# Optimization experiments

Measured on AMD Instinct MI355X. Metric: run time of the kernel, lower is better.

Reference implementation:

```python
import jax, jax.numpy as jnp
import numpy as np

N, E, F, H = 50000, 500000, 128, 128   # nodes, edges, in-features, hidden
L, R, B = 3, 8, 30                     # layers, relations, bases
G, C = 16, 8                           # graphs in batch, classes
EPS = 1e-5


def setup_inputs() -> dict:
    key = jax.random.key(0)
    ks = jax.random.split(key, 16)
    x = jax.random.normal(ks[0], (N, F), jnp.float32)
    edge_index = jax.random.randint(ks[1], (2, E), 0, N)
    edge_attr = jax.random.randint(ks[2], (E,), 0, R)
    batch = jnp.sort(jax.random.randint(ks[3], (N,), 0, G))
    # RGCN params (all layers share shapes since F == H)
    basis = jax.random.normal(ks[4], (L, B, H, H), jnp.float32) * 0.05
    comp = jax.random.normal(ks[5], (L, R, B), jnp.float32) * 0.2
    root = jax.random.normal(ks[6], (L, H, H), jnp.float32) * 0.05
    bias = jnp.zeros((L, H), jnp.float32)
    # BatchNorm (eval mode: running stats)
    bn1_gamma = jnp.ones((F,), jnp.float32)
    bn1_beta = jnp.zeros((F,), jnp.float32)
    bn1_mean = jax.random.normal(ks[7], (F,), jnp.float32) * 0.1
    bn1_var = jax.random.uniform(ks[8], (F,), jnp.float32, 0.5, 1.5)
    bn2_gamma = jnp.ones((H,), jnp.float32)
    bn2_beta = jnp.zeros((H,), jnp.float32)
    bn2_mean = jax.random.normal(ks[9], (H,), jnp.float32) * 0.1
    bn2_var = jax.random.uniform(ks[10], (H,), jnp.float32, 0.5, 1.5)
    fc1_w = jax.random.normal(ks[11], (H, H), jnp.float32) * 0.05
    fc1_b = jnp.zeros((H,), jnp.float32)
    fc2_w = jax.random.normal(ks[12], (H, C), jnp.float32) * 0.05
    fc2_b = jnp.zeros((C,), jnp.float32)
    return dict(x=x, edge_index=edge_index, edge_attr=edge_attr, batch=batch,
                bn1_gamma=bn1_gamma, bn1_beta=bn1_beta, bn1_mean=bn1_mean, bn1_var=bn1_var,
                basis=basis, comp=comp, root=root, bias=bias,
                bn2_gamma=bn2_gamma, bn2_beta=bn2_beta, bn2_mean=bn2_mean, bn2_var=bn2_var,
                fc1_w=fc1_w, fc1_b=fc1_b, fc2_w=fc2_w, fc2_b=fc2_b)


def _bn(x, gamma, beta, mean, var):
    return (x - mean) * jax.lax.rsqrt(var + EPS) * gamma + beta


def _rgcn_layer(x, basis_l, comp_l, root_l, bias_l, src, dst, edge_attr):
    # root transform + bias
    out = x @ root_l + bias_l
    # relation-wise basis-decomposed message passing, mean-aggregated per relation
    for r in range(R):
        W_r = jnp.einsum('b,bio->io', comp_l[r], basis_l)  # [H, H]
        xw = x @ W_r                                       # [N, H]
        mask = (edge_attr == r).astype(x.dtype)            # [E]
        msg = xw[src] * mask[:, None]                      # gather + mask
        agg = jax.ops.segment_sum(msg, dst, num_segments=N)
        deg = jax.ops.segment_sum(mask, dst, num_segments=N)
        out = out + agg / jnp.maximum(deg, 1.0)[:, None]
    return out


def reference(x, edge_index, edge_attr, batch,
              bn1_gamma, bn1_beta, bn1_mean, bn1_var,
              basis, comp, root, bias,
              bn2_gamma, bn2_beta, bn2_mean, bn2_var,
              fc1_w, fc1_b, fc2_w, fc2_b):
    src, dst = edge_index[0], edge_index[1]
    h = _bn(x, bn1_gamma, bn1_beta, bn1_mean, bn1_var)
    for l in range(L):
        h = jax.nn.relu(_rgcn_layer(h, basis[l], comp[l], root[l], bias[l], src, dst, edge_attr))
        # dropout is identity in eval mode
    # global mean pool per graph
    sums = jax.ops.segment_sum(h, batch, num_segments=G)            # [G, H]
    counts = jax.ops.segment_sum(jnp.ones((N,), h.dtype), batch, num_segments=G)
    g = sums / jnp.maximum(counts, 1.0)[:, None]
    g = _bn(g, bn2_gamma, bn2_beta, bn2_mean, bn2_var)
    # temporal_type == 'mean'
    v = jax.nn.relu(g.mean(axis=0))                                 # [H]
    v = jax.nn.relu(v @ fc1_w + fc1_b)
    logits = v @ fc2_w + fc2_b                                      # [C]
    return jax.nn.log_softmax(logits, axis=-1)
```

## Files before the change

### kernel.cpp

```cpp
#include <hip/hip_runtime.h>
#include <hip/hip_bf16.h>

#define NN 50000
#define NE 500000
#define HID 128
#define LAYERS 3
#define RELS 8
#define BASES 30
#define GRAPHS 16
#define CLASSES 8
#define EPSV 1e-5f
#define NOUT (HID * (RELS + 1))
#define SCAN_CHUNK 1024
#define SCAN_NBLK ((NN + SCAN_CHUNK - 1) / SCAN_CHUNK)
#define PCHUNK 128
#define NSTRIPE ((NN + 127) / 128)
#define NSG ((NSTRIPE + 7) / 8)

typedef __attribute__((ext_vector_type(8))) short short8;
typedef __attribute__((ext_vector_type(4))) float f32x4;
typedef __attribute__((ext_vector_type(2))) float f32x2;

__device__ __forceinline__ float bf2f(unsigned short u) {
    union { unsigned int i; float f; } x; x.i = ((unsigned int)u) << 16; return x.f;
}
__device__ __forceinline__ unsigned short f2bf(float f) {
    __hip_bfloat16 b = __float2bfloat16(f);
    return *(unsigned short*)&b;
}
template <bool HI>
__device__ __forceinline__ f32x2 fp8x2_2f(int u) {
    return __builtin_amdgcn_cvt_pk_f32_fp8(u, HI);
}
__device__ __forceinline__ int permf(int f) {
    return (f & 64) | ((f & 15) << 2) | ((f >> 4) & 3);
}
__device__ __forceinline__ int ipermf(int q) {
    return (q & 64) | ((q & 3) << 4) | ((q >> 2) & 15);
}
__device__ __forceinline__ void gload16(const void* g, void* l) {
    __builtin_amdgcn_global_load_lds(
        (const __attribute__((address_space(1))) unsigned int*)g,
        (__attribute__((address_space(3))) unsigned int*)l, 16, 0, 0);
}

__global__ __launch_bounds__(256) void build_wcat(const float* __restrict__ basis,
                                                  const float* __restrict__ comp,
                                                  const float* __restrict__ root,
                                                  unsigned short* __restrict__ wT) {
    int bid = blockIdx.x;
    int l = bid >> 6;
    int k0 = (bid & 63) << 1;
    __shared__ float cl[RELS * BASES];
    int tid = threadIdx.x;
    if (tid < RELS * BASES) cl[tid] = comp[l * RELS * BASES + tid];
    __syncthreads();
    int j = tid & 127;
    int k = k0 + (tid >> 7);
    int pk = permf(k);
    const float* bp = basis + ((size_t)l * BASES * HID + k) * HID + j;
    float acc[RELS];
#pragma unroll
    for (int r = 0; r < RELS; ++r) acc[r] = 0.f;
    for (int b = 0; b < BASES; ++b) {
        float v = bp[(size_t)b * HID * HID];
#pragma unroll
        for (int r = 0; r < RELS; ++r) acc[r] += cl[r * BASES + b] * v;
    }
    unsigned short* wl = wT + (size_t)l * NOUT * HID;
#pragma unroll
    for (int r = 0; r < RELS; ++r)
        wl[(size_t)((1 + r) * HID + j) * HID + pk] = f2bf(acc[r]);
    wl[(size_t)j * HID + pk] = f2bf(root[((size_t)l * HID + k) * HID + j]);
}

__global__ void bn1_kernel(const float* __restrict__ x, const float* __restrict__ gamma,
                           const float* __restrict__ beta, const float* __restrict__ mean,
                           const float* __restrict__ var, unsigned short* __restrict__ habf) {
    int idx = blockIdx.x * blockDim.x + threadIdx.x;
    if (idx >= NN * HID) return;
    int q = idx & (HID - 1);
    int n = idx >> 7;
    int f = ipermf(q);
    habf[idx] = f2bf((x[(n << 7) + f] - mean[f]) * rsqrtf(var[f] + EPSV) * gamma[f] + beta[f]);
}

__global__ void deg_kernel(const int* __restrict__ ei, const int* __restrict__ ea,
                           float* __restrict__ deg) {
    int e = blockIdx.x * blockDim.x + threadIdx.x;
    if (e >= NE) return;
    int dst = ei[NE + e];
    atomicAdd(&deg[(size_t)dst * RELS + ea[e]], 1.0f);
}

__global__ void invdeg_kernel(float* __restrict__ deg, int* __restrict__ degi) {
    int n = blockIdx.x * blockDim.x + threadIdx.x;
    if (n >= NN) return;
    float s = 0.f;
#pragma unroll
    for (int r = 0; r < RELS; ++r) {
        float d = deg[(size_t)n * RELS + r];
        s += d;
        deg[(size_t)n * RELS + r] = 1.0f / fmaxf(d, 1.0f);
    }
    degi[n] = (int)(s + 0.5f);
}

__global__ __launch_bounds__(256) void scan_partial(const int* __restrict__ degi,
                                                    int* __restrict__ rowptr,
                                                    int* __restrict__ bsum) {
    __shared__ int ssc[256];
    int t = threadIdx.x;
    int base = blockIdx.x * SCAN_CHUNK + t * 4;
    int v[4];
#pragma unroll
    for (int j = 0; j < 4; ++j) v[j] = (base + j < NN) ? degi[base + j] : 0;
    int tsum = v[0] + v[1] + v[2] + v[3];
    ssc[t] = tsum;
    __syncthreads();
    for (int ofs = 1; ofs < 256; ofs <<= 1) {
        int add = (t >= ofs) ? ssc[t - ofs] : 0;
        __syncthreads();
        ssc[t] += add;
        __syncthreads();
    }
    int excl = ssc[t] - tsum;
    int e = 0;
#pragma unroll
    for (int j = 0; j < 4; ++j) {
        if (base + j < NN) rowptr[base + j] = excl + e;
        e += v[j];
    }
    if (t == 255) bsum[blockIdx.x] = ssc[255];
}

__global__ void scan_bsum(int* __restrict__ bsum) {
    if (threadIdx.x == 0) {
        int acc = 0;
        for (int b = 0; b < SCAN_NBLK; ++b) { int v = bsum[b]; bsum[b] = acc; acc += v; }
    }
}

__global__ __launch_bounds__(256) void scan_add(int* __restrict__ rowptr,
                                                const int* __restrict__ bsum) {
    int i = blockIdx.x * blockDim.x + threadIdx.x;
    if (i < NN) rowptr[i] += bsum[i >> 10];
    if (i == 0) rowptr[NN] = NE;
}

__global__ void fill_kernel(const int* __restrict__ ei, const int* __restrict__ ea,
                            const int* __restrict__ rowptr,
                            int* __restrict__ fillcnt, int* __restrict__ epk) {
    int e = blockIdx.x * blockDim.x + threadIdx.x;
    if (e >= NE) return;
    int src = ei[e];
    int dst = ei[NE + e];
    int r = ea[e];
    int pos = atomicAdd(&fillcnt[dst], 1);
    epk[rowptr[dst] + pos] = src | (r << 20);
}

__global__ __launch_bounds__(256) void gemm_mfma(const unsigned short* __restrict__ habf,
                                                 const unsigned short* __restrict__ wT,
                                                 const float* __restrict__ bias,
                                                 unsigned short* __restrict__ hnb,
                                                 unsigned char* __restrict__ xwb) {
    __shared__ __align__(16) unsigned short As[128 * HID];
    __shared__ __align__(16) unsigned short Bs[128 * HID];
    int bid = blockIdx.x;
    int sm8 = bid & 7;
    int rest = bid >> 3;
    int n0 = rest % (RELS + 1);
    int g = rest / (RELS + 1);
    int stripe = g * 8 + sm8;
    if (stripe >= NSTRIPE) return;
    int row0 = stripe * 128;

    int tid = threadIdx.x;
    int wave = tid >> 6, lane = tid & 63;
    int wm = (wave & 1) * 64, wn = (wave >> 1) * 64;
    int quad = lane >> 4, l16 = lane & 15;

    int sr = lane >> 4;
    int sp = lane & 15;
#pragma unroll
    for (int q = 0; q < 8; ++q) {
        int rb = wave * 32 + q * 4;
        int r = rb + sr;
        int sc = (sp ^ (r & 7)) << 3;
        int ga = row0 + r; if (ga > NN - 1) ga = NN - 1;
        gload16(habf + (size_t)ga * HID + sc, &As[rb * HID]);
        gload16(wT + (size_t)(n0 * 128 + r) * HID + sc, &Bs[rb * HID]);
    }

    f32x4 acc[4][4];
#pragma unroll
    for (int i = 0; i < 4; ++i)
#pragma unroll
        for (int j = 0; j < 4; ++j) acc[i][j] = (f32x4){0.f, 0.f, 0.f, 0.f};

    __syncthreads();

    int sx = l16 & 7;
#pragma unroll
    for (int kc = 0; kc < 4; ++kc) {
        int ca = ((kc * 4 + quad) ^ sx) << 3;
        short8 a[4], b[4];
#pragma unroll
        for (int i = 0; i < 4; ++i) {
            a[i] = *(const short8*)&As[(wm + i * 16 + l16) * HID + ca];
            b[i] = *(const short8*)&Bs[(wn + i * 16 + l16) * HID + ca];
        }
#pragma unroll
        for (int i = 0; i < 4; ++i)
#pragma unroll
            for (int j = 0; j < 4; ++j)
                acc[i][j] = __builtin_amdgcn_mfma_f32_16x16x32_bf16(a[i], b[j], acc[i][j], 0, 0, 0);
    }

    int pbase = wn + l16 * 4;
    if (n0 == 0) {
#pragma unroll
        for (int i = 0; i < 4; ++i)
#pragma unroll
            for (int reg = 0; reg < 4; ++reg) {
                int grow = row0 + wm + i * 16 + quad * 4 + reg;
                if (grow >= NN) continue;
                unsigned lo = (unsigned)f2bf(acc[i][0][reg] + bias[wn + l16]) |
                              ((unsigned)f2bf(acc[i][1][reg] + bias[wn + 16 + l16]) << 16);
                unsigned hi = (unsigned)f2bf(acc[i][2][reg] + bias[wn + 32 + l16]) |
                              ((unsigned)f2bf(acc[i][3][reg] + bias[wn + 48 + l16]) << 16);
                uint2 pk = {lo, hi};
                *(uint2*)(hnb + (size_t)grow * HID + pbase) = pk;
            }
    } else {
        int cbase = (n0 - 1) * 128;
#pragma unroll
        for (int i = 0; i < 4; ++i)
#pragma unroll
            for (int reg = 0; reg < 4; ++reg) {
                int grow = row0 + wm + i * 16 + quad * 4 + reg;
                if (grow >= NN) continue;
                unsigned w = (unsigned)__builtin_amdgcn_cvt_pk_fp8_f32(acc[i][0][reg], acc[i][1][reg], 0, false);
                w = (unsigned)__builtin_amdgcn_cvt_pk_fp8_f32(acc[i][2][reg], acc[i][3][reg], (int)w, true);
                *(unsigned*)(xwb + (size_t)grow * (RELS * HID) + cbase + pbase) = w;
            }
    }
}

__global__ __launch_bounds__(256) void aggregate_kernel(const int* __restrict__ rowptr,
                                                        const int* __restrict__ epk,
                                                        const float* __restrict__ invdeg,
                                                        const unsigned char* __restrict__ xwb,
                                                        const unsigned short* __restrict__ hnb,
                                                        unsigned short* __restrict__ habf) {
    int lane = threadIdx.x & 63;
    int half = lane >> 5;
    int hl = lane & 31;
    int node = (blockIdx.x << 3) + ((threadIdx.x >> 6) << 1) + half;
    if (node >= NN) return;
    int beg = rowptr[node], end = rowptr[node + 1];
    float dv = invdeg[(size_t)node * RELS + (hl & 7)];
    float a0 = 0.f, a1 = 0.f, a2 = 0.f, a3 = 0.f;
    for (int b0 = beg; b0 < end; b0 += 32) {
        int cnt = min(32, end - b0);
        int myp = 0;
        if (hl < cnt) myp = epk[b0 + hl];
        int sbase = half << 5;
        int j = 0;
        for (; j + 4 <= cnt; j += 4) {
            int p0 = __shfl(myp, sbase + j);
            int p1 = __shfl(myp, sbase + j + 1);
            int p2 = __shfl(myp, sbase + j + 2);
            int p3 = __shfl(myp, sbase + j + 3);
            float s0 = __shfl(dv, sbase + (p0 >> 20));
            float s1 = __shfl(dv, sbase + (p1 >> 20));
            float s2 = __shfl(dv, sbase + (p2 >> 20));
            float s3 = __shfl(dv, sbase + (p3 >> 20));
            unsigned u0 = *(const unsigned*)(xwb + (size_t)(p0 & 0xFFFFF) * (RELS * HID) + (p0 >> 20) * HID + hl * 4);
            unsigned u1 = *(const unsigned*)(xwb + (size_t)(p1 & 0xFFFFF) * (RELS * HID) + (p1 >> 20) * HID + hl * 4);
            unsigned u2 = *(const unsigned*)(xwb + (size_t)(p2 & 0xFFFFF) * (RELS * HID) + (p2 >> 20) * HID + hl * 4);
            unsigned u3 = *(const unsigned*)(xwb + (size_t)(p3 & 0xFFFFF) * (RELS * HID) + (p3 >> 20) * HID + hl * 4);
            f32x2 l0 = fp8x2_2f<false>((int)u0), h0 = fp8x2_2f<true>((int)u0);
            f32x2 l1 = fp8x2_2f<false>((int)u1), h1 = fp8x2_2f<true>((int)u1);
            f32x2 l2 = fp8x2_2f<false>((int)u2), h2 = fp8x2_2f<true>((int)u2);
            f32x2 l3 = fp8x2_2f<false>((int)u3), h3 = fp8x2_2f<true>((int)u3);
            a0 += l0.x * s0 + l1.x * s1 + l2.x * s2 + l3.x * s3;
            a1 += l0.y * s0 + l1.y * s1 + l2.y * s2 + l3.y * s3;
            a2 += h0.x * s0 + h1.x * s1 + h2.x * s2 + h3.x * s3;
            a3 += h0.y * s0 + h1.y * s1 + h2.y * s2 + h3.y * s3;
        }
        for (; j < cnt; ++j) {
            int p = __shfl(myp, sbase + j);
            float s = __shfl(dv, sbase + (p >> 20));
            unsigned u = *(const unsigned*)(xwb + (size_t)(p & 0xFFFFF) * (RELS * HID) + (p >> 20) * HID + hl * 4);
            f32x2 lo = fp8x2_2f<false>((int)u), hi = fp8x2_2f<true>((int)u);
            a0 += lo.x * s; a1 += lo.y * s; a2 += hi.x * s; a3 += hi.y * s;
        }
    }
    const ushort2* hp = (const ushort2*)(hnb + (size_t)node * HID + hl * 4);
    ushort2 c0 = hp[0], c1 = hp[1];
    ushort2 o0, o1;
    o0.x = f2bf(fmaxf(bf2f(c0.x) + a0, 0.f));
    o0.y = f2bf(fmaxf(bf2f(c0.y) + a1, 0.f));
    o1.x = f2bf(fmaxf(bf2f(c1.x) + a2, 0.f));
    o1.y = f2bf(fmaxf(bf2f(c1.y) + a3, 0.f));
    ushort2* op = (ushort2*)(habf + (size_t)node * HID + hl * 4);
    op[0] = o0;
    op[1] = o1;
}

__global__ __launch_bounds__(256) void pool_kernel(const unsigned short* __restrict__ habf,
                                                   const int* __restrict__ batch,
                                                   float* __restrict__ psum,
                                                   float* __restrict__ pcnt) {
    int tid = threadIdx.x;
    int f = tid & 127;
    int sub = tid >> 7;
    int base = blockIdx.x * PCHUNK;
    float acc = 0.f, cnt = 0.f;
    int gcur = -1;
    for (int it = 0; it < PCHUNK / 2; ++it) {
        int node = base + it * 2 + sub;
        if (node >= NN) break;
        int g = batch[node];
        if (g != gcur) {
            if (gcur >= 0) {
                atomicAdd(&psum[gcur * HID + f], acc);
                if (f == 0) atomicAdd(&pcnt[gcur], cnt);
            }
            gcur = g; acc = 0.f; cnt = 0.f;
        }
        acc += bf2f(habf[(size_t)node * HID + f]);
        cnt += 1.f;
    }
    if (gcur >= 0) {
        atomicAdd(&psum[gcur * HID + f], acc);
        if (f == 0) atomicAdd(&pcnt[gcur], cnt);
    }
}

__global__ void head_kernel(const float* __restrict__ psum, const float* __restrict__ pcnt,
                            const float* __restrict__ g2, const float* __restrict__ b2,
                            const float* __restrict__ m2, const float* __restrict__ v2,
                            const float* __restrict__ fc1w, const float* __restrict__ fc1b,
                            const float* __restrict__ fc2w, const float* __restrict__ fc2b,
                            float* __restrict__ out) {
    __shared__ float v[HID];
    __shared__ float u[HID];
    __shared__ float lg[CLASSES];
    int j = threadIdx.x;
    int pj = permf(j);
    float acc = 0.f;
    for (int g = 0; g < GRAPHS; ++g) {
        float val = psum[g * HID + pj] / fmaxf(pcnt[g], 1.0f);
        val = (val - m2[j]) * rsqrtf(v2[j] + EPSV) * g2[j] + b2[j];
        acc += val;
    }
    v[j] = fmaxf(acc / (float)GRAPHS, 0.f);
    __syncthreads();
    float s = fc1b[j];
    for (int k = 0; k < HID; ++k) s += v[k] * fc1w[k * HID + j];
    u[j] = fmaxf(s, 0.f);
    __syncthreads();
    if (j < CLASSES) {
        float t = fc2b[j];
        for (int k = 0; k < HID; ++k) t += u[k] * fc2w[k * CLASSES + j];
        lg[j] = t;
    }
    __syncthreads();
    if (j < CLASSES) {
        float mx = lg[0];
        for (int c = 1; c < CLASSES; ++c) mx = fmaxf(mx, lg[c]);
        float se = 0.f;
        for (int c = 0; c < CLASSES; ++c) se += expf(lg[c] - mx);
        out[j] = lg[j] - mx - logf(se);
    }
}

extern "C" void kernel_launch(void* const* d_in, const int* in_sizes, int n_in,
                              void* d_out, int out_size, void* d_ws, size_t ws_size,
                              hipStream_t stream) {
    const float* x     = (const float*)d_in[0];
    const int*   ei    = (const int*)d_in[1];
    const int*   ea    = (const int*)d_in[2];
    const int*   batch = (const int*)d_in[3];
    const float* bn1g  = (const float*)d_in[4];
    const float* bn1b  = (const float*)d_in[5];
    const float* bn1m  = (const float*)d_in[6];
    const float* bn1v  = (const float*)d_in[7];
    const float* basis = (const float*)d_in[8];
    const float* comp  = (const float*)d_in[9];
    const float* root  = (const float*)d_in[10];
    const float* bias  = (const float*)d_in[11];
    const float* bn2g  = (const float*)d_in[12];
    const float* bn2b  = (const float*)d_in[13];
    const float* bn2m  = (const float*)d_in[14];
    const float* bn2v  = (const float*)d_in[15];
    const float* fc1w  = (const float*)d_in[16];
    const float* fc1b  = (const float*)d_in[17];
    const float* fc2w  = (const float*)d_in[18];
    const float* fc2b  = (const float*)d_in[19];

    float* ws = (float*)d_ws;
    size_t off = 0;
    unsigned short* wT = (unsigned short*)(ws + off); off += (size_t)LAYERS * NOUT * HID / 2;
    unsigned short* hnb  = (unsigned short*)(ws + off); off += (size_t)NN * HID / 2;
    unsigned short* habf = (unsigned short*)(ws + off); off += (size_t)NN * HID / 2;
    float* deg    = ws + off; off += (size_t)NN * RELS;
    float* psum   = ws + off; off += (size_t)GRAPHS * HID + GRAPHS;
    float* pcnt   = psum + GRAPHS * HID;
    int* degi     = (int*)(ws + off); off += (size_t)NN;
    int* rowptr   = (int*)(ws + off); off += (size_t)NN + 1;
    int* fillcnt  = (int*)(ws + off); off += (size_t)NN;
    int* bsum     = (int*)(ws + off); off += (size_t)SCAN_NBLK;
    int* epk      = (int*)(ws + off); off += (size_t)NE;
    off = (off + 3) & ~(size_t)3;
    unsigned char* xwb = (unsigned char*)(ws + off);
    off += (size_t)NN * RELS * HID / 4;
    if (ws_size < off * sizeof(float)) return;

    hipMemsetAsync(psum, 0, (GRAPHS * HID + GRAPHS) * sizeof(float), stream);
    hipMemsetAsync(deg, 0, (size_t)NN * RELS * sizeof(float), stream);
    hipMemsetAsync(fillcnt, 0, (size_t)NN * sizeof(int), stream);

    build_wcat<<<LAYERS * 64, 256, 0, stream>>>(basis, comp, root, wT);
    bn1_kernel<<<(NN * HID + 255) / 256, 256, 0, stream>>>(x, bn1g, bn1b, bn1m, bn1v, habf);

    deg_kernel<<<(NE + 255) / 256, 256, 0, stream>>>(ei, ea, deg);
    invdeg_kernel<<<(NN + 255) / 256, 256, 0, stream>>>(deg, degi);
    scan_partial<<<SCAN_NBLK, 256, 0, stream>>>(degi, rowptr, bsum);
    scan_bsum<<<1, 64, 0, stream>>>(bsum);
    scan_add<<<(NN + 255) / 256, 256, 0, stream>>>(rowptr, bsum);
    fill_kernel<<<(NE + 255) / 256, 256, 0, stream>>>(ei, ea, rowptr, fillcnt, epk);

    int gblocks = NSG * (RELS + 1) * 8;
    for (int l = 0; l < LAYERS; ++l) {
        gemm_mfma<<<gblocks, 256, 0, stream>>>(habf, wT + (size_t)l * NOUT * HID,
                                               bias + (size_t)l * HID, hnb, xwb);
        aggregate_kernel<<<(NN + 7) / 8, 256, 0, stream>>>(rowptr, epk, deg, xwb, hnb, habf);
    }

    pool_kernel<<<(NN + PCHUNK - 1) / PCHUNK, 256, 0, stream>>>(habf, batch, psum, pcnt);
    head_kernel<<<1, 128, 0, stream>>>(psum, pcnt, bn2g, bn2b, bn2m, bn2v,
                                       fc1w, fc1b, fc2w, fc2b, (float*)d_out);
}
```

Baseline: 406.9 us.

## Split GEMM K-loop to halve LDS, fuse invdeg into scan, unroll aggregate by 8

The GEMM kernel now stages A and B in two K-halves of 64 columns, which halves shared memory per block so more blocks can be resident, at the cost of extra barriers and less load/compute overlap within a block. The inverse-degree computation is folded into the scan_partial kernel, removing one launch and the degi buffer, though each scan thread now reads the 8 relation degrees of its nodes with a strided pattern. The aggregate gather loop is unrolled from 4 to 8 edges so more independent fp8 loads are in flight, which raises register pressure.

```diff
diff --git a/kernel.cpp b/kernel.cpp
--- a/kernel.cpp
+++ b/kernel.cpp
@@ -93,20 +93,7 @@
     atomicAdd(&deg[(size_t)dst * RELS + ea[e]], 1.0f);
 }
 
-__global__ void invdeg_kernel(float* __restrict__ deg, int* __restrict__ degi) {
-    int n = blockIdx.x * blockDim.x + threadIdx.x;
-    if (n >= NN) return;
-    float s = 0.f;
-#pragma unroll
-    for (int r = 0; r < RELS; ++r) {
-        float d = deg[(size_t)n * RELS + r];
-        s += d;
-        deg[(size_t)n * RELS + r] = 1.0f / fmaxf(d, 1.0f);
-    }
-    degi[n] = (int)(s + 0.5f);
-}
-
-__global__ __launch_bounds__(256) void scan_partial(const int* __restrict__ degi,
+__global__ __launch_bounds__(256) void scan_partial(float* __restrict__ deg,
                                                     int* __restrict__ rowptr,
                                                     int* __restrict__ bsum) {
     __shared__ int ssc[256];
@@ -114,7 +101,19 @@
     int base = blockIdx.x * SCAN_CHUNK + t * 4;
     int v[4];
 #pragma unroll
-    for (int j = 0; j < 4; ++j) v[j] = (base + j < NN) ? degi[base + j] : 0;
+    for (int j = 0; j < 4; ++j) {
+        int node = base + j;
+        if (node < NN) {
+            float s = 0.f;
+#pragma unroll
+            for (int r = 0; r < RELS; ++r) {
+                float d = deg[(size_t)node * RELS + r];
+                s += d;
+                deg[(size_t)node * RELS + r] = 1.0f / fmaxf(d, 1.0f);
+            }
+            v[j] = (int)(s + 0.5f);
+        } else v[j] = 0;
+    }
     int tsum = v[0] + v[1] + v[2] + v[3];
     ssc[t] = tsum;
     __syncthreads();
@@ -165,8 +164,8 @@
                                                  const float* __restrict__ bias,
                                                  unsigned short* __restrict__ hnb,
                                                  unsigned char* __restrict__ xwb) {
-    __shared__ __align__(16) unsigned short As[128 * HID];
-    __shared__ __align__(16) unsigned short Bs[128 * HID];
+    __shared__ __align__(16) unsigned short As[128 * 64];
+    __shared__ __align__(16) unsigned short Bs[128 * 64];
     int bid = blockIdx.x;
     int sm8 = bid & 7;
     int rest = bid >> 3;
@@ -181,41 +180,44 @@
     int wm = (wave & 1) * 64, wn = (wave >> 1) * 64;
     int quad = lane >> 4, l16 = lane & 15;
 
-    int sr = lane >> 4;
-    int sp = lane & 15;
-#pragma unroll
-    for (int q = 0; q < 8; ++q) {
-        int rb = wave * 32 + q * 4;
-        int r = rb + sr;
-        int sc = (sp ^ (r & 7)) << 3;
-        int ga = row0 + r; if (ga > NN - 1) ga = NN - 1;
-        gload16(habf + (size_t)ga * HID + sc, &As[rb * HID]);
-        gload16(wT + (size_t)(n0 * 128 + r) * HID + sc, &Bs[rb * HID]);
-    }
-
     f32x4 acc[4][4];
 #pragma unroll
     for (int i = 0; i < 4; ++i)
 #pragma unroll
         for (int j = 0; j < 4; ++j) acc[i][j] = (f32x4){0.f, 0.f, 0.f, 0.f};
 
-    __syncthreads();
-
+    int lr = lane >> 3;
+    int lc = lane & 7;
     int sx = l16 & 7;
-#pragma unroll
-    for (int kc = 0; kc < 4; ++kc) {
-        int ca = ((kc * 4 + quad) ^ sx) << 3;
-        short8 a[4], b[4];
-#pragma unroll
-        for (int i = 0; i < 4; ++i) {
-            a[i] = *(const short8*)&As[(wm + i * 16 + l16) * HID + ca];
-            b[i] = *(const short8*)&Bs[(wn + i * 16 + l16) * HID + ca];
-        }
-#pragma unroll
-        for (int i = 0; i < 4; ++i)
-#pragma unroll
-            for (int j = 0; j < 4; ++j)
-                acc[i][j] = __builtin_amdgcn_mfma_f32_16x16x32_bf16(a[i], b[j], acc[i][j], 0, 0, 0);
+
+#pragma unroll
+    for (int kh = 0; kh < 2; ++kh) {
+#pragma unroll
+        for (int q = 0; q < 4; ++q) {
+            int rb = wave * 32 + q * 8;
+            int r = rb + lr;
+            int sc = (lc ^ (r & 7)) << 3;
+            int ga = row0 + r; if (ga > NN - 1) ga = NN - 1;
+            gload16(habf + (size_t)ga * HID + kh * 64 + sc, &As[rb * 64]);
+            gload16(wT + (size_t)(n0 * 128 + r) * HID + kh * 64 + sc, &Bs[rb * 64]);
+        }
+        __syncthreads();
+#pragma unroll
+        for (int kc = 0; kc < 2; ++kc) {
+            int ca = ((kc * 4 + quad) ^ sx) << 3;
+            short8 a[4], b[4];
+#pragma unroll
+            for (int i = 0; i < 4; ++i) {
+                a[i] = *(const short8*)&As[(wm + i * 16 + l16) * 64 + ca];
+                b[i] = *(const short8*)&Bs[(wn + i * 16 + l16) * 64 + ca];
+            }
+#pragma unroll
+            for (int i = 0; i < 4; ++i)
+#pragma unroll
+                for (int j = 0; j < 4; ++j)
+                    acc[i][j] = __builtin_amdgcn_mfma_f32_16x16x32_bf16(a[i], b[j], acc[i][j], 0, 0, 0);
+        }
+        __syncthreads();
     }
 
     int pbase = wn + l16 * 4;
@@ -262,33 +264,42 @@
     int beg = rowptr[node], end = rowptr[node + 1];
     float dv = invdeg[(size_t)node * RELS + (hl & 7)];
     float a0 = 0.f, a1 = 0.f, a2 = 0.f, a3 = 0.f;
+    int sbase = half << 5;
     for (int b0 = beg; b0 < end; b0 += 32) {
         int cnt = min(32, end - b0);
         int myp = 0;
         if (hl < cnt) myp = epk[b0 + hl];
-        int sbase = half << 5;
         int j = 0;
-        for (; j + 4 <= cnt; j += 4) {
-            int p0 = __shfl(myp, sbase + j);
-            int p1 = __shfl(myp, sbase + j + 1);
-            int p2 = __shfl(myp, sbase + j + 2);
-            int p3 = __shfl(myp, sbase + j + 3);
-            float s0 = __shfl(dv, sbase + (p0 >> 20));
-            float s1 = __shfl(dv, sbase + (p1 >> 20));
-            float s2 = __shfl(dv, sbase + (p2 >> 20));
-            float s3 = __shfl(dv, sbase + (p3 >> 20));
-            unsigned u0 = *(const unsigned*)(xwb + (size_t)(p0 & 0xFFFFF) * (RELS * HID) + (p0 >> 20) * HID + hl * 4);
-            unsigned u1 = *(const unsigned*)(xwb + (size_t)(p1 & 0xFFFFF) * (RELS * HID) + (p1 >> 20) * HID + hl * 4);
-            unsigned u2 = *(const unsigned*)(xwb + (size_t)(p2 & 0xFFFFF) * (RELS * HID) + (p2 >> 20) * HID + hl * 4);
-            unsigned u3 = *(const unsigned*)(xwb + (size_t)(p3 & 0xFFFFF) * (RELS * HID) + (p3 >> 20) * HID + hl * 4);
-            f32x2 l0 = fp8x2_2f<false>((int)u0), h0 = fp8x2_2f<true>((int)u0);
-            f32x2 l1 = fp8x2_2f<false>((int)u1), h1 = fp8x2_2f<true>((int)u1);
-            f32x2 l2 = fp8x2_2f<false>((int)u2), h2 = fp8x2_2f<true>((int)u2);
-            f32x2 l3 = fp8x2_2f<false>((int)u3), h3 = fp8x2_2f<true>((int)u3);
-            a0 += l0.x * s0 + l1.x * s1 + l2.x * s2 + l3.x * s3;
-            a1 += l0.y * s0 + l1.y * s1 + l2.y * s2 + l3.y * s3;
-            a2 += h0.x * s0 + h1.x * s1 + h2.x * s2 + h3.x * s3;
-            a3 += h0.y * s0 + h1.y * s1 + h2.y * s2 + h3.y * s3;
+        for (; j + 8 <= cnt; j += 8) {
+            int p[8]; float s[8]; unsigned u[8];
+#pragma unroll
+            for (int t = 0; t < 8; ++t) p[t] = __shfl(myp, sbase + j + t);
+#pragma unroll
+            for (int t = 0; t < 8; ++t) s[t] = __shfl(dv, sbase + (p[t] >> 20));
+#pragma unroll
+            for (int t = 0; t < 8; ++t)
+                u[t] = *(const unsigned*)(xwb + (size_t)(p[t] & 0xFFFFF) * (RELS * HID) + (p[t] >> 20) * HID + hl * 4);
+#pragma unroll
+            for (int t = 0; t < 8; ++t) {
+                f32x2 lo = fp8x2_2f<false>((int)u[t]), hi = fp8x2_2f<true>((int)u[t]);
+                a0 += lo.x * s[t]; a1 += lo.y * s[t]; a2 += hi.x * s[t]; a3 += hi.y * s[t];
+            }
+        }
+        if (j + 4 <= cnt) {
+            int p[4]; float s[4]; unsigned u[4];
+#pragma unroll
+            for (int t = 0; t < 4; ++t) p[t] = __shfl(myp, sbase + j + t);
+#pragma unroll
+            for (int t = 0; t < 4; ++t) s[t] = __shfl(dv, sbase + (p[t] >> 20));
+#pragma unroll
+            for (int t = 0; t < 4; ++t)
+                u[t] = *(const unsigned*)(xwb + (size_t)(p[t] & 0xFFFFF) * (RELS * HID) + (p[t] >> 20) * HID + hl * 4);
+#pragma unroll
+            for (int t = 0; t < 4; ++t) {
+                f32x2 lo = fp8x2_2f<false>((int)u[t]), hi = fp8x2_2f<true>((int)u[t]);
+                a0 += lo.x * s[t]; a1 += lo.y * s[t]; a2 += hi.x * s[t]; a3 += hi.y * s[t];
+            }
+            j += 4;
         }
         for (; j < cnt; ++j) {
             int p = __shfl(myp, sbase + j);
@@ -410,7 +421,6 @@
     float* deg    = ws + off; off += (size_t)NN * RELS;
     float* psum   = ws + off; off += (size_t)GRAPHS * HID + GRAPHS;
     float* pcnt   = psum + GRAPHS * HID;
-    int* degi     = (int*)(ws + off); off += (size_t)NN;
     int* rowptr   = (int*)(ws + off); off += (size_t)NN + 1;
     int* fillcnt  = (int*)(ws + off); off += (size_t)NN;
     int* bsum     = (int*)(ws + off); off += (size_t)SCAN_NBLK;
@@ -428,8 +438,7 @@
     bn1_kernel<<<(NN * HID + 255) / 256, 256, 0, stream>>>(x, bn1g, bn1b, bn1m, bn1v, habf);
 
     deg_kernel<<<(NE + 255) / 256, 256, 0, stream>>>(ei, ea, deg);
-    invdeg_kernel<<<(NN + 255) / 256, 256, 0, stream>>>(deg, degi);
-    scan_partial<<<SCAN_NBLK, 256, 0, stream>>>(degi, rowptr, bsum);
+    scan_partial<<<SCAN_NBLK, 256, 0, stream>>>(deg, rowptr, bsum);
     scan_bsum<<<1, 64, 0, stream>>>(bsum);
     scan_add<<<(NN + 255) / 256, 256, 0, stream>>>(rowptr, bsum);
     fill_kernel<<<(NE + 255) / 256, 256, 0, stream>>>(ei, ea, rowptr, fillcnt, epk);
```

Measured after the change: 397.1 us (median of 2 runs). 1.02x faster.
